# Performance work log

Measured on AMD Instinct MI355X. Metric: run time of the kernel, lower is better.

Reference implementation:

```python
import jax, jax.numpy as jnp
import numpy as np

# Model constants (match init_kwargs)
H = 16       # num query heads
HKV = 8      # num kv heads
G = H // HKV # group size for GQA
D = 128      # head_dim
EPS = 1e-06
THETA = 10000.0
SCALE = D ** -0.5


def setup_inputs() -> dict:
    key = jax.random.key(0)
    k1, k2, k3 = jax.random.split(key, 3)
    T, HID = 2048, 2048
    qkv_out = H * D + 2 * HKV * D  # 4096
    return {
        "x": jax.random.normal(k1, (T, HID), jnp.float32),
        "pos": jnp.arange(T, dtype=jnp.int64 if jax.config.jax_enable_x64 else jnp.int32),
        "w_qkv": jax.random.normal(k2, (HID, qkv_out), jnp.float32) * 0.02,
        "q_norm_w": jnp.ones((D,), jnp.float32),
        "k_norm_w": jnp.ones((D,), jnp.float32),
        "w_o": jax.random.normal(k3, (H * D, HID), jnp.float32) * 0.02,
    }


def _rmsnorm(x, w):
    # per-head RMSNorm over last dim (head_dim)
    var = jnp.mean(jnp.square(x), axis=-1, keepdims=True)
    return x * jax.lax.rsqrt(var + EPS) * w


def _rope(x, pos):
    # neox-style rotary: rotate_half over full head_dim
    inv_freq = 1.0 / (THETA ** (jnp.arange(0, D, 2, dtype=jnp.float32) / D))  # [D/2]
    ang = pos.astype(jnp.float32)[:, None] * inv_freq                          # [T, D/2]
    cos = jnp.concatenate([jnp.cos(ang), jnp.cos(ang)], -1)[:, None, :]        # [T,1,D]
    sin = jnp.concatenate([jnp.sin(ang), jnp.sin(ang)], -1)[:, None, :]
    x1, x2 = x[..., : D // 2], x[..., D // 2 :]
    rot = jnp.concatenate([-x2, x1], -1)
    return x * cos + rot * sin


def reference(x, pos, w_qkv, q_norm_w, k_norm_w, w_o):
    T = x.shape[0]
    qkv = x @ w_qkv                                   # [T, (H+2*HKV)*D]
    q = qkv[:, : H * D].reshape(T, H, D)
    k = qkv[:, H * D : (H + HKV) * D].reshape(T, HKV, D)
    v = qkv[:, (H + HKV) * D :].reshape(T, HKV, D)
    q = _rmsnorm(q, q_norm_w)
    k = _rmsnorm(k, k_norm_w)
    q = _rope(q, pos)
    k = _rope(k, pos)
    # GQA causal attention over a single flattened sequence
    qg = q.reshape(T, HKV, G, D)
    scores = jnp.einsum("qhgd,khd->hgqk", qg, k) * SCALE   # [HKV,G,T,T]
    causal = pos[:, None] >= pos[None, :]                   # [T,T]
    scores = jnp.where(causal, scores, jnp.finfo(scores.dtype).min)
    probs = jax.nn.softmax(scores, axis=-1)
    o = jnp.einsum("hgqk,khd->qhgd", probs, v).reshape(T, H * D)
    return o @ w_o
```

## Files before the change

kernel.cpp:

```cpp
#include <hip/hip_runtime.h>
#include <hip/hip_bf16.h>
#include <math.h>

#define T_SEQ 2048
#define HID   2048
#define NH    16
#define NKV   8
#define DH    128
#define QKV_N 4096
#define KOFF  2048
#define VOFF  3072
#define EPS_RMS 1e-6f
#define ATT_SCALE 0.08838834764831845f

typedef __attribute__((ext_vector_type(8))) short bf16x8;
typedef __attribute__((ext_vector_type(4))) float f32x4;
typedef unsigned short u16;

__device__ __forceinline__ u16 f2b(float f) {
  union { float f; unsigned u; } v; v.f = f;
  unsigned r = v.u + 0x7fff + ((v.u >> 16) & 1);
  return (u16)(r >> 16);
}
__device__ __forceinline__ float b2f(u16 x) {
  union { unsigned u; float f; } v; v.u = ((unsigned)x) << 16;
  return v.f;
}

__device__ __forceinline__ void g2l16(u16* l, const u16* g) {
#if __has_builtin(__builtin_amdgcn_global_load_lds)
  __builtin_amdgcn_global_load_lds(
      (const __attribute__((address_space(1))) unsigned int*)g,
      (__attribute__((address_space(3))) unsigned int*)l, 16, 0, 0);
#else
  *(float4*)l = *(const float4*)g;
#endif
}

__global__ __launch_bounds__(256)
void cast_bf16(const float* __restrict__ src, u16* __restrict__ dst) {
  const int i = blockIdx.x * 256 + threadIdx.x;
  const float4 v = ((const float4*)src)[i];
  ushort4 o; o.x = f2b(v.x); o.y = f2b(v.y); o.z = f2b(v.z); o.w = f2b(v.w);
  ((ushort4*)dst)[i] = o;
}

__global__ __launch_bounds__(256)
void tcast(const float* __restrict__ src, u16* __restrict__ dst, int R, int C) {
  __shared__ u16 tile[32][36];
  const int br = blockIdx.y * 32, bc = blockIdx.x * 32;
  const int t = threadIdx.x;
  {
    const int r = t >> 3, c4 = (t & 7) * 4;
    const float4 v = *(const float4*)(src + (size_t)(br + r) * C + bc + c4);
    tile[c4 + 0][r] = f2b(v.x);
    tile[c4 + 1][r] = f2b(v.y);
    tile[c4 + 2][r] = f2b(v.z);
    tile[c4 + 3][r] = f2b(v.w);
  }
  __syncthreads();
  {
    const int c = t >> 3, r4 = (t & 7) * 4;
    ushort4 o = { tile[c][r4], tile[c][r4 + 1], tile[c][r4 + 2], tile[c][r4 + 3] };
    *(ushort4*)(dst + (size_t)(bc + c) * R + br + r4) = o;
  }
}

template<int BOUT>
__global__ __launch_bounds__(256)
void gemm_bt(const u16* __restrict__ A, const u16* __restrict__ BT,
             void* __restrict__ Cout, int M, int N, int K) {
  __shared__ u16 sA[128 * 32];
  __shared__ u16 sB[128 * 32];

  const int t = threadIdx.x;
  const int lane = t & 63, wv = t >> 6;
  const int lo = lane & 15, hi = lane >> 4;
  const int bm = blockIdx.y * 128, bn = blockIdx.x * 128;
  const int wr = (wv >> 1) * 64, wc = (wv & 1) * 64;

  f32x4 acc[4][4];
#pragma unroll
  for (int m = 0; m < 4; ++m)
#pragma unroll
    for (int n = 0; n < 4; ++n) acc[m][n] = (f32x4){0.f, 0.f, 0.f, 0.f};

  const int arow = wv * 32 + (lane >> 2);
  const int koff = (lane & 3) * 8;
  const u16* gA = A + (size_t)(bm + arow) * K + koff;
  const u16* gB = BT + (size_t)(bn + arow) * K + koff;
  u16* lA = sA + wv * 1024 + lane * 8;
  u16* lB = sB + wv * 1024 + lane * 8;

  for (int k0 = 0; k0 < K; k0 += 32) {
    g2l16(lA,       gA + k0);
    g2l16(lA + 512, gA + (size_t)16 * K + k0);
    g2l16(lB,       gB + k0);
    g2l16(lB + 512, gB + (size_t)16 * K + k0);
    __syncthreads();

    bf16x8 af[4], bfr[4];
#pragma unroll
    for (int m = 0; m < 4; ++m)
      af[m] = *(const bf16x8*)(sA + (wr + m * 16 + lo) * 32 + hi * 8);
#pragma unroll
    for (int n = 0; n < 4; ++n)
      bfr[n] = *(const bf16x8*)(sB + (wc + n * 16 + lo) * 32 + hi * 8);
#pragma unroll
    for (int m = 0; m < 4; ++m)
#pragma unroll
      for (int n = 0; n < 4; ++n)
        acc[m][n] = __builtin_amdgcn_mfma_f32_16x16x32_bf16(af[m], bfr[n], acc[m][n], 0, 0, 0);
    __syncthreads();
  }

#pragma unroll
  for (int m = 0; m < 4; ++m)
#pragma unroll
    for (int n = 0; n < 4; ++n)
#pragma unroll
      for (int r = 0; r < 4; ++r) {
        const int row = bm + wr + m * 16 + hi * 4 + r;
        const int col = bn + wc + n * 16 + lo;
        if constexpr (BOUT)
          ((u16*)Cout)[(size_t)row * N + col] = f2b(acc[m][n][r]);
        else
          ((float*)Cout)[(size_t)row * N + col] = acc[m][n][r];
      }
}

__global__ __launch_bounds__(256)
void normrope(const u16* __restrict__ qkvb, const int* __restrict__ pos,
              const float* __restrict__ qw, const float* __restrict__ kw,
              u16* __restrict__ qbf, u16* __restrict__ kbf) {
  const int wv = threadIdx.x >> 6, lane = threadIdx.x & 63;
  const int idx = blockIdx.x * 4 + wv;
  const int tt = idx / 24, hh = idx % 24;

  const int off = (hh < NH) ? hh * DH : KOFF + (hh - NH) * DH;
  const u16* base = qkvb + (size_t)tt * QKV_N + off;
  const float x1 = b2f(base[lane]);
  const float x2 = b2f(base[lane + 64]);

  float ss = x1 * x1 + x2 * x2;
#pragma unroll
  for (int o = 32; o > 0; o >>= 1) ss += __shfl_xor(ss, o);

  const float inv = rsqrtf(ss * (1.0f / DH) + EPS_RMS);
  const float* w = (hh < NH) ? qw : kw;
  const float n1 = x1 * inv * w[lane];
  const float n2 = x2 * inv * w[lane + 64];

  const float p    = (float)pos[tt];
  const float freq = powf(10000.0f, -(float)lane * (1.0f / 64.0f));
  const float ang  = p * freq;
  const float c = cosf(ang), s = sinf(ang);
  const float o1 = n1 * c - n2 * s;
  const float o2 = n2 * c + n1 * s;

  if (hh < NH) {
    u16* dst = qbf + ((size_t)tt * NH + hh) * DH;
    dst[lane]      = f2b(o1);
    dst[lane + 64] = f2b(o2);
  } else {
    const int u = (tt & 7) << 3;
    u16* dst = kbf + ((size_t)tt * NKV + (hh - NH)) * DH;
    dst[lane ^ u]        = f2b(o1);
    dst[(lane ^ u) + 64] = f2b(o2);
  }
}

__global__ __launch_bounds__(256)
void vtrans(const u16* __restrict__ qkvb, u16* __restrict__ vT) {
  __shared__ u16 td[128][40];
  const int kvh = blockIdx.y;
  const int t0  = blockIdx.x * 32;
  const int f   = threadIdx.x;
  {
    const int r = f >> 3, c0 = (f & 7) * 16;
    const u16* src = qkvb + (size_t)(t0 + r) * QKV_N + VOFF + kvh * DH + c0;
    bf16x8 a = *(const bf16x8*)src;
    bf16x8 b = *(const bf16x8*)(src + 8);
#pragma unroll
    for (int j = 0; j < 8; ++j) td[c0 + j][r]     = ((u16*)&a)[j];
#pragma unroll
    for (int j = 0; j < 8; ++j) td[c0 + 8 + j][r] = ((u16*)&b)[j];
  }
  __syncthreads();
  {
    const int d = f >> 1, half = f & 1;
    const int sw = (d & 7) << 3;
    u16* orow = vT + (size_t)(kvh * DH + d) * T_SEQ;
#pragma unroll
    for (int g = 0; g < 2; ++g) {
      const int tb = t0 + half * 16 + g * 8;
      *(bf16x8*)(orow + (tb ^ sw)) = *(const bf16x8*)(&td[d][half * 16 + g * 8]);
    }
  }
}

__global__ __launch_bounds__(256)
void flash_mfma(const u16* __restrict__ qbf, const u16* __restrict__ kbf,
                const u16* __restrict__ vT, u16* __restrict__ obuf) {
  __shared__ u16 kls[64 * 128];
  __shared__ u16 vls[128 * 64];
  __shared__ u16 pls[4][16][72];

  const int t = threadIdx.x, lane = t & 63, wv = t >> 6;
  const int lo = lane & 15, hi = lane >> 4;
  const int h = blockIdx.y, kvh = h >> 1;
  const int qt = gridDim.x - 1 - blockIdx.x;
  const int q0 = qt * 64;

  bf16x8 qf[4];
#pragma unroll
  for (int kk = 0; kk < 4; ++kk)
    qf[kk] = *(const bf16x8*)(qbf + ((size_t)(q0 + wv * 16 + lo) * NH + h) * DH
                              + kk * 32 + hi * 8);

  f32x4 oacc[8];
#pragma unroll
  for (int n = 0; n < 8; ++n) oacc[n] = (f32x4){0.f, 0.f, 0.f, 0.f};
  float mrow[4] = {-INFINITY, -INFINITY, -INFINITY, -INFINITY};
  float lrow[4] = {0.f, 0.f, 0.f, 0.f};

  for (int kt = 0; kt <= qt; ++kt) {
    const int k0 = kt * 64;
#pragma unroll
    for (int c = 0; c < 4; ++c) {
      const int chunk = wv * 4 + c;
      const int krow  = chunk * 4 + (lane >> 4);
      g2l16(kls + chunk * 512 + lane * 8,
            kbf + ((size_t)(k0 + krow) * NKV + kvh) * DH + lo * 8);
      const int d = chunk * 8 + (lane >> 3);
      g2l16(vls + chunk * 512 + lane * 8,
            vT + (size_t)(kvh * DH + d) * T_SEQ + k0 + (lane & 7) * 8);
    }
    __syncthreads();

    f32x4 sacc[4];
#pragma unroll
    for (int n = 0; n < 4; ++n) sacc[n] = (f32x4){0.f, 0.f, 0.f, 0.f};
#pragma unroll
    for (int n = 0; n < 4; ++n) {
      const int r = n * 16 + lo;
      const u16* kb = kls + r * 128;
#pragma unroll
      for (int kk = 0; kk < 4; ++kk) {
        const int offs = (kk * 32 + hi * 8) ^ ((r & 7) << 3);
        bf16x8 b = *(const bf16x8*)(kb + offs);
        sacc[n] = __builtin_amdgcn_mfma_f32_16x16x32_bf16(qf[kk], b, sacc[n], 0, 0, 0);
      }
    }

    float pv[4][4], tm[4];
    const bool diag = (kt == qt);
#pragma unroll
    for (int r = 0; r < 4; ++r) {
      const int qi = q0 + wv * 16 + hi * 4 + r;
      float mx = -INFINITY;
#pragma unroll
      for (int n = 0; n < 4; ++n) {
        float s = sacc[n][r] * ATT_SCALE;
        if (diag && qi < k0 + n * 16 + lo) s = -INFINITY;
        pv[n][r] = s;
        mx = fmaxf(mx, s);
      }
      tm[r] = mx;
    }
#pragma unroll
    for (int o = 8; o > 0; o >>= 1)
#pragma unroll
      for (int r = 0; r < 4; ++r) tm[r] = fmaxf(tm[r], __shfl_xor(tm[r], o));

    float al[4], rs[4];
#pragma unroll
    for (int r = 0; r < 4; ++r) {
      const float mn = fmaxf(mrow[r], tm[r]);
      al[r] = __expf(mrow[r] - mn);
      mrow[r] = mn;
      rs[r] = 0.f;
    }
#pragma unroll
    for (int n = 0; n < 4; ++n)
#pragma unroll
      for (int r = 0; r < 4; ++r) {
        const float p = __expf(pv[n][r] - mrow[r]);
        pv[n][r] = p;
        rs[r] += p;
      }
#pragma unroll
    for (int o = 8; o > 0; o >>= 1)
#pragma unroll
      for (int r = 0; r < 4; ++r) rs[r] += __shfl_xor(rs[r], o);
#pragma unroll
    for (int r = 0; r < 4; ++r) lrow[r] = lrow[r] * al[r] + rs[r];
#pragma unroll
    for (int n = 0; n < 8; ++n)
#pragma unroll
      for (int r = 0; r < 4; ++r) oacc[n][r] *= al[r];

#pragma unroll
    for (int n = 0; n < 4; ++n)
#pragma unroll
      for (int r = 0; r < 4; ++r)
        pls[wv][hi * 4 + r][n * 16 + lo] = f2b(pv[n][r]);

    bf16x8 pa[2];
#pragma unroll
    for (int kk = 0; kk < 2; ++kk)
      pa[kk] = *(const bf16x8*)(&pls[wv][lo][kk * 32 + hi * 8]);
#pragma unroll
    for (int n = 0; n < 8; ++n) {
      const int d = n * 16 + lo;
      const u16* vb = vls + d * 64;
#pragma unroll
      for (int kk = 0; kk < 2; ++kk) {
        const int offs = (kk * 32 + hi * 8) ^ ((d & 7) << 3);
        bf16x8 b = *(const bf16x8*)(vb + offs);
        oacc[n] = __builtin_amdgcn_mfma_f32_16x16x32_bf16(pa[kk], b, oacc[n], 0, 0, 0);
      }
    }
    __syncthreads();
  }

  float inv[4];
#pragma unroll
  for (int r = 0; r < 4; ++r) inv[r] = 1.0f / lrow[r];
#pragma unroll
  for (int n = 0; n < 8; ++n)
#pragma unroll
    for (int r = 0; r < 4; ++r)
      obuf[(size_t)(q0 + wv * 16 + hi * 4 + r) * HID + h * DH + n * 16 + lo] =
          f2b(oacc[n][r] * inv[r]);
}

extern "C" void kernel_launch(void* const* d_in, const int* in_sizes, int n_in,
                              void* d_out, int out_size, void* d_ws, size_t ws_size,
                              hipStream_t stream) {
  const float* x     = (const float*)d_in[0];
  const int*   pos   = (const int*)d_in[1];
  const float* w_qkv = (const float*)d_in[2];
  const float* qw    = (const float*)d_in[3];
  const float* kw    = (const float*)d_in[4];
  const float* w_o   = (const float*)d_in[5];
  float* out = (float*)d_out;

  char* w = (char*)d_ws;
  u16* xbf   = (u16*)w;
  u16* qbf   = xbf;
  u16* wqkvT = (u16*)(w + 8388608);
  u16* kbf   = wqkvT;
  u16* vTb   = wqkvT + 2097152;
  u16* obuf  = wqkvT + 4194304;
  u16* woT   = (u16*)(w + 25165824);
  u16* qkvbf = (u16*)(w + 33554432);

  cast_bf16<<<T_SEQ * HID / 4 / 256, 256, 0, stream>>>(x, xbf);
  tcast<<<dim3(QKV_N / 32, HID / 32), 256, 0, stream>>>(w_qkv, wqkvT, HID, QKV_N);
  tcast<<<dim3(HID / 32, HID / 32), 256, 0, stream>>>(w_o, woT, HID, HID);

  gemm_bt<1><<<dim3(QKV_N / 128, T_SEQ / 128), 256, 0, stream>>>(
      xbf, wqkvT, qkvbf, T_SEQ, QKV_N, HID);

  normrope<<<T_SEQ * 24 / 4, 256, 0, stream>>>(qkvbf, pos, qw, kw, qbf, kbf);
  vtrans<<<dim3(T_SEQ / 32, NKV), 256, 0, stream>>>(qkvbf, vTb);

  flash_mfma<<<dim3(T_SEQ / 64, NH), 256, 0, stream>>>(qbf, kbf, vTb, obuf);

  gemm_bt<0><<<dim3(HID / 128, T_SEQ / 128), 256, 0, stream>>>(
      obuf, woT, out, T_SEQ, HID, HID);
}
```

Before: 327.2 us.

## Overlap K/V tile loads with compute in flash attention and remap blocks to XCDs

The flash attention loop now issues the next K tile load right after the QK MFMAs and the next V tile load right after the PV MFMAs. The goal is to overlap global-to-LDS traffic with softmax and matmul work instead of stalling at the top of each iteration. The grid is flattened to 1D and decoded so that both query heads sharing a KV head run on the same XCD, which should improve L2 reuse of K/V. It also adds s_setprio around the MFMA sections and replaces powf with exp2f for the RoPE frequency. These add extra syncs per iteration and tie the block mapping to a fixed grid size.

```diff
diff --git a/kernel.cpp b/kernel.cpp
--- a/kernel.cpp
+++ b/kernel.cpp
@@ -152,7 +152,7 @@
   const float n2 = x2 * inv * w[lane + 64];
 
   const float p    = (float)pos[tt];
-  const float freq = powf(10000.0f, -(float)lane * (1.0f / 64.0f));
+  const float freq = exp2f((float)lane * -0.20762050593046014f);
   const float ang  = p * freq;
   const float c = cosf(ang), s = sinf(ang);
   const float o1 = n1 * c - n2 * s;
@@ -208,9 +208,14 @@
 
   const int t = threadIdx.x, lane = t & 63, wv = t >> 6;
   const int lo = lane & 15, hi = lane >> 4;
-  const int h = blockIdx.y, kvh = h >> 1;
-  const int qt = gridDim.x - 1 - blockIdx.x;
-  const int q0 = qt * 64;
+
+  const int id  = blockIdx.x;
+  const int xcd = id & 7;
+  const int idx = id >> 3;
+  const int h   = xcd * 2 + (idx & 1);
+  const int qt  = 31 - (idx >> 1);
+  const int kvh = h >> 1;
+  const int q0  = qt * 64;
 
   bf16x8 qf[4];
 #pragma unroll
@@ -224,23 +229,35 @@
   float mrow[4] = {-INFINITY, -INFINITY, -INFINITY, -INFINITY};
   float lrow[4] = {0.f, 0.f, 0.f, 0.f};
 
-  for (int kt = 0; kt <= qt; ++kt) {
-    const int k0 = kt * 64;
+  auto stage_k = [&](int k0) {
 #pragma unroll
     for (int c = 0; c < 4; ++c) {
       const int chunk = wv * 4 + c;
-      const int krow  = chunk * 4 + (lane >> 4);
       g2l16(kls + chunk * 512 + lane * 8,
-            kbf + ((size_t)(k0 + krow) * NKV + kvh) * DH + lo * 8);
+            kbf + ((size_t)(k0 + chunk * 4 + hi) * NKV + kvh) * DH + lo * 8);
+    }
+  };
+  auto stage_v = [&](int k0) {
+#pragma unroll
+    for (int c = 0; c < 4; ++c) {
+      const int chunk = wv * 4 + c;
       const int d = chunk * 8 + (lane >> 3);
       g2l16(vls + chunk * 512 + lane * 8,
             vT + (size_t)(kvh * DH + d) * T_SEQ + k0 + (lane & 7) * 8);
     }
-    __syncthreads();
+  };
+
+  stage_k(0);
+  stage_v(0);
+  __syncthreads();
+
+  for (int kt = 0; kt <= qt; ++kt) {
+    const int k0 = kt * 64;
 
     f32x4 sacc[4];
 #pragma unroll
     for (int n = 0; n < 4; ++n) sacc[n] = (f32x4){0.f, 0.f, 0.f, 0.f};
+    __builtin_amdgcn_s_setprio(1);
 #pragma unroll
     for (int n = 0; n < 4; ++n) {
       const int r = n * 16 + lo;
@@ -252,6 +269,10 @@
         sacc[n] = __builtin_amdgcn_mfma_f32_16x16x32_bf16(qf[kk], b, sacc[n], 0, 0, 0);
       }
     }
+    __builtin_amdgcn_s_setprio(0);
+
+    __syncthreads();
+    if (kt < qt) stage_k(k0 + 64);
 
     float pv[4][4], tm[4];
     const bool diag = (kt == qt);
@@ -310,6 +331,7 @@
 #pragma unroll
     for (int kk = 0; kk < 2; ++kk)
       pa[kk] = *(const bf16x8*)(&pls[wv][lo][kk * 32 + hi * 8]);
+    __builtin_amdgcn_s_setprio(1);
 #pragma unroll
     for (int n = 0; n < 8; ++n) {
       const int d = n * 16 + lo;
@@ -321,7 +343,10 @@
         oacc[n] = __builtin_amdgcn_mfma_f32_16x16x32_bf16(pa[kk], b, oacc[n], 0, 0, 0);
       }
     }
+    __builtin_amdgcn_s_setprio(0);
+
     __syncthreads();
+    if (kt < qt) stage_v(k0 + 64);
   }
 
   float inv[4];
@@ -366,7 +391,7 @@
   normrope<<<T_SEQ * 24 / 4, 256, 0, stream>>>(qkvbf, pos, qw, kw, qbf, kbf);
   vtrans<<<dim3(T_SEQ / 32, NKV), 256, 0, stream>>>(qkvbf, vTb);
 
-  flash_mfma<<<dim3(T_SEQ / 64, NH), 256, 0, stream>>>(qbf, kbf, vTb, obuf);
+  flash_mfma<<<dim3(T_SEQ / 64 * NH), 256, 0, stream>>>(qbf, kbf, vTb, obuf);
 
   gemm_bt<0><<<dim3(HID / 128, T_SEQ / 128), 256, 0, stream>>>(
       obuf, woT, out, T_SEQ, HID, HID);
```

Measured after the change: 302.2 us. 7.7% less time.
